# Kernel tuning notes

Hardware: AMD Instinct MI355X
Metric: run time of the kernel (lower is better)

The kernel has to match this reference:

```python
import jax, jax.numpy as jnp
import numpy as np

LATENT = 64

def _linear(x, W, b):
    return x @ W.T + b

def setup_inputs() -> dict:
    key = jax.random.key(0)
    ks = jax.random.split(key, 16)
    B, D, H, L = 16384, 784, 1024, LATENT
    def u(k, shape, fan_in):
        bound = 1.0 / np.sqrt(fan_in)
        return jax.random.uniform(k, shape, jnp.float32, -bound, bound)
    inp = {
        "x": jax.random.uniform(ks[0], (B, D), jnp.float32),
        "epsilon": jax.random.normal(ks[1], (B, L), jnp.float32),
        "W_ih": u(ks[2], (H, D), D), "b_ih": u(ks[3], (H,), D),
        "W_m":  u(ks[4], (L, H), H), "b_m":  u(ks[5], (L,), H),
        "W_lv": u(ks[6], (L, H), H), "b_lv": u(ks[7], (L,), H),
        "W_ap": u(ks[8], (L, H), H), "b_ap": u(ks[9], (L,), H),
        "W_lh": u(ks[10], (H, L), L), "b_lh": u(ks[11], (H,), L),
        "W_ho": u(ks[12], (D, H), H), "b_ho": u(ks[13], (D,), H),
    }
    return inp

def reference(x, epsilon, W_ih, b_ih, W_m, b_m, W_lv, b_lv, W_ap, b_ap, W_lh, b_lh, W_ho, b_ho):
    # ----- encode -----
    hidden = jnp.tanh(_linear(x, W_ih, b_ih))            # [B,H]
    mean   = _linear(hidden, W_m, b_m)                   # [B,L]
    logvar = jnp.clip(_linear(hidden, W_lv, b_lv), -4.5, 0.0)  # Hardtanh(-4.5,0)
    approx = _linear(hidden, W_ap, b_ap)                 # [B,L]
    # ----- reparameterize (rank-1 Gaussian) -----
    # inv_cov = diag(exp(logvar)) + approx approx^T   per sample
    B, L = mean.shape
    eye = jnp.eye(L, dtype=mean.dtype)
    inv_cov = jnp.exp(logvar)[:, :, None] * eye + approx[:, :, None] * approx[:, None, :]  # [B,L,L]
    cov = jnp.linalg.inv(inv_cov)                        # batched 64x64 inverse
    # torch.potrf default returns UPPER Cholesky U with U^T U = cov -> U = chol(cov).T
    Sigma = jnp.swapaxes(jnp.linalg.cholesky(cov), -1, -2)  # [B,L,L] upper
    z = mean + jnp.einsum('bij,bj->bi', Sigma, epsilon)  # [B,L]
    # ----- decode -----
    h2 = jnp.tanh(_linear(z, W_lh, b_lh))
    x_mean = jax.nn.sigmoid(_linear(h2, W_ho, b_ho))     # [B,784]
    return (x_mean, z, mean, logvar, approx)
```

## Files before the change

### kernel.cpp

```cpp
#include <hip/hip_runtime.h>
#include <hip/hip_bf16.h>
#include <math.h>

typedef __attribute__((ext_vector_type(8))) short short8;
typedef __attribute__((ext_vector_type(4))) float f32x4;
typedef __attribute__((ext_vector_type(4))) unsigned short us4;

#define GLOBAL_AS __attribute__((address_space(1)))
#define LDS_AS __attribute__((address_space(3)))

__device__ inline void g2l16(const void* g, void* l) {
    __builtin_amdgcn_global_load_lds((const GLOBAL_AS void*)g, (LDS_AS void*)l, 16, 0, 0);
}

__device__ inline unsigned short f2bf(float f) {
    unsigned int u = __float_as_uint(f);
    return (unsigned short)((u + 0x7fffu + ((u >> 16) & 1u)) >> 16);
}

template <int EPI>
__global__ __launch_bounds__(512, 2) void mgemm8(
    const __hip_bfloat16* __restrict__ A,
    const __hip_bfloat16* __restrict__ W,
    const float* __restrict__ bias,
    void* __restrict__ outp,
    int lda, int ldb, int nT, int ldc, int Nreal)
{
    __shared__ __align__(16) __hip_bfloat16 sh[2][32768];

    const int tid  = threadIdx.x;
    const int wave = tid >> 6;
    const int lane = tid & 63;
    const int rBase = blockIdx.x * 256;
    const int cBase = blockIdx.y * 256;

    const __hip_bfloat16* Ab = A + (size_t)rBase * lda;
    const __hip_bfloat16* Wb = W + (size_t)cBase * ldb;

    const int wr = (wave >> 2) * 128;
    const int wc = (wave & 3) * 64;
    const int h  = lane >> 4;
    const int r0 = lane & 15;
    const int swz = h ^ ((r0 >> 1) & 3);

    f32x4 acc[8][4];
#pragma unroll
    for (int m = 0; m < 8; ++m)
#pragma unroll
        for (int n = 0; n < 4; ++n) acc[m][n] = (f32x4){0.f, 0.f, 0.f, 0.f};

    auto stage_half = [&](int bb, int t, int ks) {
        const int k0 = t * 64 + ks * 32;
#pragma unroll
        for (int r = 0; r < 2; ++r) {
            int s2  = r * 512 + tid;
            int row = s2 >> 2;
            int cg  = (s2 & 3) ^ ((row >> 1) & 3);
            g2l16(Ab + (size_t)row * lda + k0 + cg * 8,
                  &sh[bb][(ks * 1024 + s2) * 8]);
            g2l16(Wb + (size_t)row * ldb + k0 + cg * 8,
                  &sh[bb][16384 + (ks * 1024 + s2) * 8]);
        }
    };

    auto phase = [&](int bb, int ks) {
        const __hip_bfloat16* base = &sh[bb][ks * 1024 * 8];
        short8 a_[8], b_[4];
#pragma unroll
        for (int i = 0; i < 8; ++i) {
            int R = wr + i * 16 + r0;
            a_[i] = *(const short8*)(base + (R * 4 + swz) * 8);
        }
#pragma unroll
        for (int j = 0; j < 4; ++j) {
            int R = wc + j * 16 + r0;
            b_[j] = *(const short8*)(base + 16384 + (R * 4 + swz) * 8);
        }
        __builtin_amdgcn_s_setprio(1);
#pragma unroll
        for (int i = 0; i < 8; ++i)
#pragma unroll
            for (int j = 0; j < 4; ++j)
                acc[i][j] = __builtin_amdgcn_mfma_f32_16x16x32_bf16(a_[i], b_[j], acc[i][j], 0, 0, 0);
        __builtin_amdgcn_s_setprio(0);
    };

    stage_half(0, 0, 0);
    stage_half(0, 0, 1);
    stage_half(1, 1, 0);
    for (int t = 0; t < nT; ++t) {
        const int cur = t & 1;
        if (t + 1 < nT) asm volatile("s_waitcnt vmcnt(8)" ::: "memory");
        else            asm volatile("s_waitcnt vmcnt(4)" ::: "memory");
        __builtin_amdgcn_s_barrier();
        if (t + 1 < nT) stage_half(cur ^ 1, t + 1, 1);
        phase(cur, 0);
        if (t + 1 < nT) asm volatile("s_waitcnt vmcnt(8)" ::: "memory");
        else            asm volatile("s_waitcnt vmcnt(0)" ::: "memory");
        __builtin_amdgcn_s_barrier();
        if (t + 2 < nT) stage_half(cur, t + 2, 0);
        phase(cur, 1);
    }

    const int rq = lane >> 4;
    const int c0 = lane & 15;
#pragma unroll
    for (int m = 0; m < 8; ++m) {
#pragma unroll
        for (int n = 0; n < 4; ++n) {
            f32x4 v = acc[m][n];
            const int gc = cBase + wc + n * 16 + c0;
            const float bv = bias[gc];
#pragma unroll
            for (int j = 0; j < 4; ++j) {
                const int gr = rBase + wr + m * 16 + rq * 4 + j;
                float val = v[j] + bv;
                if (EPI == 1) {
                    ((__hip_bfloat16*)outp)[(size_t)gr * ldc + gc] = __float2bfloat16(tanhf(val));
                } else {
                    if (gc < Nreal)
                        ((float*)outp)[(size_t)gr * Nreal + gc] = 1.f / (1.f + expf(-val));
                }
            }
        }
    }
}

template <int EPI>
__global__ __launch_bounds__(256) void mgemm(
    const __hip_bfloat16* __restrict__ A,
    const __hip_bfloat16* __restrict__ W,
    const float* __restrict__ bias,
    void* __restrict__ outp,
    int lda, int ldb, int nT, int ldc, int Nreal)
{
    __shared__ __align__(16) __hip_bfloat16 sh[2][8192];

    const int tid  = threadIdx.x;
    const int wave = tid >> 6;
    const int lane = tid & 63;
    const int rBase = blockIdx.x * 128;
    const int cBase = blockIdx.y * 128;

    const __hip_bfloat16* Ab = A + (size_t)rBase * lda;
    const __hip_bfloat16* Wb = W + (size_t)cBase * ldb;

    const int wr = (wave >> 1) * 64;
    const int wc = (wave & 1) * 64;
    const int h  = lane >> 4;
    const int r0 = lane & 15;
    const int swz = h ^ ((r0 >> 1) & 3);

    f32x4 acc[4][4];
#pragma unroll
    for (int m = 0; m < 4; ++m)
#pragma unroll
        for (int n = 0; n < 4; ++n) acc[m][n] = (f32x4){0.f, 0.f, 0.f, 0.f};

    auto stage = [&](int bb, int k0) {
#pragma unroll
        for (int r = 0; r < 2; ++r) {
            int s2  = r * 256 + tid;
            int row = s2 >> 2;
            int cg  = (s2 & 3) ^ ((row >> 1) & 3);
            g2l16(Ab + (size_t)row * lda + k0 + cg * 8, &sh[bb][s2 * 8]);
            g2l16(Wb + (size_t)row * ldb + k0 + cg * 8, &sh[bb][4096 + s2 * 8]);
        }
    };

    auto compute = [&](int bb) {
        const __hip_bfloat16* base = &sh[bb][0];
        short8 a_[4], b_[4];
#pragma unroll
        for (int m = 0; m < 4; ++m) {
            int R = wr + m * 16 + r0;
            a_[m] = *(const short8*)(base + (R * 4 + swz) * 8);
        }
#pragma unroll
        for (int n = 0; n < 4; ++n) {
            int R = wc + n * 16 + r0;
            b_[n] = *(const short8*)(base + 4096 + (R * 4 + swz) * 8);
        }
#pragma unroll
        for (int m = 0; m < 4; ++m)
#pragma unroll
            for (int n = 0; n < 4; ++n)
                acc[m][n] = __builtin_amdgcn_mfma_f32_16x16x32_bf16(a_[m], b_[n], acc[m][n], 0, 0, 0);
    };

    stage(0, 0);
    __syncthreads();
    int cur = 0;
    for (int t = 0; t < nT; ++t) {
        if (t + 1 < nT) stage(cur ^ 1, (t + 1) * 32);
        compute(cur);
        __syncthreads();
        cur ^= 1;
    }

    const int rq = lane >> 4;
    const int c0 = lane & 15;
#pragma unroll
    for (int m = 0; m < 4; ++m) {
#pragma unroll
        for (int n = 0; n < 4; ++n) {
            f32x4 v = acc[m][n];
            const int gc = cBase + wc + n * 16 + c0;
            const float bv = bias[gc];
#pragma unroll
            for (int j = 0; j < 4; ++j) {
                const int gr = rBase + wr + m * 16 + rq * 4 + j;
                float val = v[j] + bv;
                if (EPI == 0) {
                    const int sel = gc >> 6, cc = gc & 63;
                    if (sel < 3) {
                        if (sel == 1) val = fminf(fmaxf(val, -4.5f), 0.f);
                        ((float*)outp)[(size_t)sel * (16384u * 64u) + (size_t)gr * 64 + cc] = val;
                    }
                } else if (EPI == 1) {
                    ((__hip_bfloat16*)outp)[(size_t)gr * ldc + gc] = __float2bfloat16(tanhf(val));
                }
            }
        }
    }
}

__global__ void cvt_pad4(const float* __restrict__ src, unsigned short* __restrict__ dst,
                         int scols, int dcols, long total4)
{
    long i = (long)blockIdx.x * 256 + threadIdx.x;
    if (i >= total4) return;
    long e = i * 4;
    long row = e / dcols;
    int  c = (int)(e - row * dcols);
    us4 o = (us4){0, 0, 0, 0};
    if (c < scols) {
        float4 v = *(const float4*)(src + row * (long)scols + c);
        o.x = f2bf(v.x); o.y = f2bf(v.y); o.z = f2bf(v.z); o.w = f2bf(v.w);
    }
    *(us4*)(dst + e) = o;
}

__global__ void cvt_rows4(const float* __restrict__ src, unsigned short* __restrict__ dst,
                          int srows, long total4)
{
    long i = (long)blockIdx.x * 256 + threadIdx.x;
    if (i >= total4) return;
    long e = i * 4;
    int r = (int)(e >> 10), c = (int)(e & 1023);
    us4 o = (us4){0, 0, 0, 0};
    if (r < srows) {
        float4 v = *(const float4*)(src + (size_t)r * 1024 + c);
        o.x = f2bf(v.x); o.y = f2bf(v.y); o.z = f2bf(v.z); o.w = f2bf(v.w);
    }
    *(us4*)(dst + e) = o;
}

__global__ void pack_heads(const float* __restrict__ Wm, const float* __restrict__ Wlv,
                           const float* __restrict__ Wap, __hip_bfloat16* __restrict__ dst)
{
    int i = blockIdx.x * 256 + threadIdx.x;
    int r = i >> 10, c = i & 1023;
    float v = 0.f;
    if (r < 64)       v = Wm[(size_t)r * 1024 + c];
    else if (r < 128) v = Wlv[(size_t)(r - 64) * 1024 + c];
    else if (r < 192) v = Wap[(size_t)(r - 128) * 1024 + c];
    dst[i] = __float2bfloat16(v);
}

__global__ void pack_bias3(const float* bm, const float* blv, const float* bap, float* dst)
{
    int i = threadIdx.x;
    float v = 0.f;
    if (i < 64)       v = bm[i];
    else if (i < 128) v = blv[i - 64];
    else if (i < 192) v = bap[i - 128];
    dst[i] = v;
}

__global__ void pad_vec(const float* src, float* dst, int n, int total)
{
    int i = blockIdx.x * 256 + threadIdx.x;
    if (i >= total) return;
    dst[i] = (i < n) ? src[i] : 0.f;
}

__global__ __launch_bounds__(256) void reparam_kernel(
    const float* __restrict__ mean, const float* __restrict__ logvar,
    const float* __restrict__ approx, const float* __restrict__ eps,
    float* __restrict__ z, __hip_bfloat16* __restrict__ zb, int B)
{
    const int gid  = blockIdx.x * 256 + threadIdx.x;
    const int row  = gid >> 6;
    const int lane = threadIdx.x & 63;
    if (row >= B) return;

    const size_t idx = (size_t)row * 64 + lane;
    const float m  = mean[idx];
    const float lv = logvar[idx];
    const float a  = approx[idx];
    const float ep = eps[idx];

    const float s  = expf(-lv);
    const float x1 = a * a * s;
    const float x2 = s * a * ep;

    float R = x1, S = x2;
#pragma unroll
    for (int off = 1; off < 64; off <<= 1) {
        float r2 = __shfl_down(R, off, 64);
        float s2 = __shfl_down(S, off, 64);
        if (lane + off < 64) { R += r2; S += s2; }
    }
    const float Rexc  = R - x1;
    const float Sexc  = S - x2;
    const float inv1R = 1.f / (1.f + R);
    const float dL    = sqrtf(s * (1.f + Rexc) * inv1R);
    const float bj    = -s * a * inv1R / dL;

    const float zv = m + dL * ep + bj * Sexc;
    z[idx]  = zv;
    zb[idx] = __float2bfloat16(zv);
}

extern "C" void kernel_launch(void* const* d_in, const int* in_sizes, int n_in,
                              void* d_out, int out_size, void* d_ws, size_t ws_size,
                              hipStream_t stream)
{
    const float* x    = (const float*)d_in[0];
    const float* eps  = (const float*)d_in[1];
    const float* W_ih = (const float*)d_in[2];
    const float* b_ih = (const float*)d_in[3];
    const float* W_m  = (const float*)d_in[4];
    const float* b_m  = (const float*)d_in[5];
    const float* W_lv = (const float*)d_in[6];
    const float* b_lv = (const float*)d_in[7];
    const float* W_ap = (const float*)d_in[8];
    const float* b_ap = (const float*)d_in[9];
    const float* W_lh = (const float*)d_in[10];
    const float* b_lh = (const float*)d_in[11];
    const float* W_ho = (const float*)d_in[12];
    const float* b_ho = (const float*)d_in[13];

    const int B = 16384;

    float* out    = (float*)d_out;
    float* x_mean = out;
    float* z      = out + (size_t)B * 784;
    float* mean   = z + (size_t)B * 64;
    float* logvar = mean + (size_t)B * 64;
    float* approx = logvar + (size_t)B * 64;

    char* ws = (char*)d_ws;
    __hip_bfloat16* hb    = (__hip_bfloat16*)(ws + 0);
    __hip_bfloat16* xb    = (__hip_bfloat16*)(ws + 33554432);
    __hip_bfloat16* wihb  = (__hip_bfloat16*)(ws + 60817408);
    __hip_bfloat16* whead = (__hip_bfloat16*)(ws + 62521344);
    __hip_bfloat16* wlhb  = (__hip_bfloat16*)(ws + 63045632);
    __hip_bfloat16* whob  = (__hip_bfloat16*)(ws + 63176704);
    float*          bhead = (float*)(ws + 65273856);
    float*          bho   = (float*)(ws + 65274880);
    __hip_bfloat16* h2b   = hb;
    __hip_bfloat16* zb    = xb;

    long g;
    g = (long)B * 832 / 4;
    cvt_pad4<<<dim3((g + 255) / 256), dim3(256), 0, stream>>>(x, (unsigned short*)xb, 784, 832, g);
    g = 1024L * 832 / 4;
    cvt_pad4<<<dim3((g + 255) / 256), dim3(256), 0, stream>>>(W_ih, (unsigned short*)wihb, 784, 832, g);
    pack_heads<<<dim3(1024), dim3(256), 0, stream>>>(W_m, W_lv, W_ap, whead);
    pack_bias3<<<dim3(1), dim3(256), 0, stream>>>(b_m, b_lv, b_ap, bhead);
    g = 1024L * 64 / 4;
    cvt_pad4<<<dim3((g + 255) / 256), dim3(256), 0, stream>>>(W_lh, (unsigned short*)wlhb, 64, 64, g);
    g = 1024L * 1024 / 4;
    cvt_rows4<<<dim3((g + 255) / 256), dim3(256), 0, stream>>>(W_ho, (unsigned short*)whob, 784, g);
    pad_vec<<<dim3(4), dim3(256), 0, stream>>>(b_ho, bho, 784, 1024);

    mgemm8<1><<<dim3(64, 4), dim3(512), 0, stream>>>(xb, wihb, b_ih, hb, 832, 832, 13, 1024, 1024);

    mgemm<0><<<dim3(128, 2), dim3(256), 0, stream>>>(hb, whead, bhead, mean, 1024, 1024, 32, 0, 192);

    reparam_kernel<<<dim3((B * 64) / 256), dim3(256), 0, stream>>>(mean, logvar, approx, eps, z, zb, B);

    mgemm<1><<<dim3(128, 8), dim3(256), 0, stream>>>(zb, wlhb, b_lh, h2b, 64, 64, 2, 1024, 1024);

    mgemm8<2><<<dim3(64, 4), dim3(512), 0, stream>>>(h2b, whob, bho, x_mean, 1024, 1024, 16, 784, 784);
}
```

Baseline: 167.0 us.

## Shrink GEMM tiles to 256x128 with K=32 stages and trim decoder padding

Replaces the 256x256, K=64 split-phase GEMM with a 256x128 tile using K=32 double-buffered stages, 8 waves each computing 64x64, and launch bounds allowing 4 blocks per CU. The decoder output GEMM now pads N to 896 instead of 1024, using 7 column blocks, which avoids wasted work on padded columns. The aim is better occupancy and less padding waste. In exchange, each tile reuses less data from LDS and the pipeline gains an extra barrier per iteration.

After: 160.5 us. -3.9%, faster.

```diff
diff --git a/kernel.cpp b/kernel.cpp
--- a/kernel.cpp
+++ b/kernel.cpp
@@ -19,93 +19,91 @@
 }
 
 template <int EPI>
-__global__ __launch_bounds__(512, 2) void mgemm8(
+__global__ __launch_bounds__(512, 4) void mgemmB(
     const __hip_bfloat16* __restrict__ A,
     const __hip_bfloat16* __restrict__ W,
     const float* __restrict__ bias,
     void* __restrict__ outp,
     int lda, int ldb, int nT, int ldc, int Nreal)
 {
-    __shared__ __align__(16) __hip_bfloat16 sh[2][32768];
+    __shared__ __align__(16) __hip_bfloat16 sh[2][12288];
 
     const int tid  = threadIdx.x;
     const int wave = tid >> 6;
     const int lane = tid & 63;
     const int rBase = blockIdx.x * 256;
-    const int cBase = blockIdx.y * 256;
+    const int cBase = blockIdx.y * 128;
 
     const __hip_bfloat16* Ab = A + (size_t)rBase * lda;
     const __hip_bfloat16* Wb = W + (size_t)cBase * ldb;
 
-    const int wr = (wave >> 2) * 128;
-    const int wc = (wave & 3) * 64;
+    const int wr = (wave >> 1) * 64;
+    const int wc = (wave & 1) * 64;
     const int h  = lane >> 4;
     const int r0 = lane & 15;
     const int swz = h ^ ((r0 >> 1) & 3);
 
-    f32x4 acc[8][4];
-#pragma unroll
-    for (int m = 0; m < 8; ++m)
+    f32x4 acc[4][4];
+#pragma unroll
+    for (int m = 0; m < 4; ++m)
 #pragma unroll
         for (int n = 0; n < 4; ++n) acc[m][n] = (f32x4){0.f, 0.f, 0.f, 0.f};
 
-    auto stage_half = [&](int bb, int t, int ks) {
-        const int k0 = t * 64 + ks * 32;
+    auto stage = [&](int bb, int t) {
+        const int k0 = t * 32;
 #pragma unroll
         for (int r = 0; r < 2; ++r) {
             int s2  = r * 512 + tid;
             int row = s2 >> 2;
             int cg  = (s2 & 3) ^ ((row >> 1) & 3);
-            g2l16(Ab + (size_t)row * lda + k0 + cg * 8,
-                  &sh[bb][(ks * 1024 + s2) * 8]);
-            g2l16(Wb + (size_t)row * ldb + k0 + cg * 8,
-                  &sh[bb][16384 + (ks * 1024 + s2) * 8]);
+            g2l16(Ab + (size_t)row * lda + k0 + cg * 8, &sh[bb][s2 * 8]);
+        }
+        {
+            int s2  = tid;
+            int row = s2 >> 2;
+            int cg  = (s2 & 3) ^ ((row >> 1) & 3);
+            g2l16(Wb + (size_t)row * ldb + k0 + cg * 8, &sh[bb][8192 + s2 * 8]);
         }
     };
 
-    auto phase = [&](int bb, int ks) {
-        const __hip_bfloat16* base = &sh[bb][ks * 1024 * 8];
-        short8 a_[8], b_[4];
-#pragma unroll
-        for (int i = 0; i < 8; ++i) {
-            int R = wr + i * 16 + r0;
-            a_[i] = *(const short8*)(base + (R * 4 + swz) * 8);
-        }
-#pragma unroll
-        for (int j = 0; j < 4; ++j) {
-            int R = wc + j * 16 + r0;
-            b_[j] = *(const short8*)(base + 16384 + (R * 4 + swz) * 8);
+    auto compute = [&](int bb) {
+        const __hip_bfloat16* base = &sh[bb][0];
+        short8 a_[4], b_[4];
+#pragma unroll
+        for (int m = 0; m < 4; ++m) {
+            int R = wr + m * 16 + r0;
+            a_[m] = *(const short8*)(base + (R * 4 + swz) * 8);
+        }
+#pragma unroll
+        for (int n = 0; n < 4; ++n) {
+            int R = wc + n * 16 + r0;
+            b_[n] = *(const short8*)(base + 8192 + (R * 4 + swz) * 8);
         }
         __builtin_amdgcn_s_setprio(1);
 #pragma unroll
-        for (int i = 0; i < 8; ++i)
-#pragma unroll
-            for (int j = 0; j < 4; ++j)
-                acc[i][j] = __builtin_amdgcn_mfma_f32_16x16x32_bf16(a_[i], b_[j], acc[i][j], 0, 0, 0);
+        for (int m = 0; m < 4; ++m)
+#pragma unroll
+            for (int n = 0; n < 4; ++n)
+                acc[m][n] = __builtin_amdgcn_mfma_f32_16x16x32_bf16(a_[m], b_[n], acc[m][n], 0, 0, 0);
         __builtin_amdgcn_s_setprio(0);
     };
 
-    stage_half(0, 0, 0);
-    stage_half(0, 0, 1);
-    stage_half(1, 1, 0);
+    stage(0, 0);
+    stage(1, 1);
     for (int t = 0; t < nT; ++t) {
         const int cur = t & 1;
-        if (t + 1 < nT) asm volatile("s_waitcnt vmcnt(8)" ::: "memory");
-        else            asm volatile("s_waitcnt vmcnt(4)" ::: "memory");
-        __builtin_amdgcn_s_barrier();
-        if (t + 1 < nT) stage_half(cur ^ 1, t + 1, 1);
-        phase(cur, 0);
-        if (t + 1 < nT) asm volatile("s_waitcnt vmcnt(8)" ::: "memory");
+        if (t + 1 < nT) asm volatile("s_waitcnt vmcnt(3)" ::: "memory");
         else            asm volatile("s_waitcnt vmcnt(0)" ::: "memory");
         __builtin_amdgcn_s_barrier();
-        if (t + 2 < nT) stage_half(cur, t + 2, 0);
-        phase(cur, 1);
+        compute(cur);
+        __builtin_amdgcn_s_barrier();
+        if (t + 2 < nT) stage(cur, t + 2);
     }
 
     const int rq = lane >> 4;
     const int c0 = lane & 15;
 #pragma unroll
-    for (int m = 0; m < 8; ++m) {
+    for (int m = 0; m < 4; ++m) {
 #pragma unroll
         for (int n = 0; n < 4; ++n) {
             f32x4 v = acc[m][n];
@@ -372,11 +370,11 @@
     pack_bias3<<<dim3(1), dim3(256), 0, stream>>>(b_m, b_lv, b_ap, bhead);
     g = 1024L * 64 / 4;
     cvt_pad4<<<dim3((g + 255) / 256), dim3(256), 0, stream>>>(W_lh, (unsigned short*)wlhb, 64, 64, g);
-    g = 1024L * 1024 / 4;
+    g = 896L * 1024 / 4;
     cvt_rows4<<<dim3((g + 255) / 256), dim3(256), 0, stream>>>(W_ho, (unsigned short*)whob, 784, g);
-    pad_vec<<<dim3(4), dim3(256), 0, stream>>>(b_ho, bho, 784, 1024);
-
-    mgemm8<1><<<dim3(64, 4), dim3(512), 0, stream>>>(xb, wihb, b_ih, hb, 832, 832, 13, 1024, 1024);
+    pad_vec<<<dim3(4), dim3(256), 0, stream>>>(b_ho, bho, 784, 896);
+
+    mgemmB<1><<<dim3(64, 8), dim3(512), 0, stream>>>(xb, wihb, b_ih, hb, 832, 832, 26, 1024, 1024);
 
     mgemm<0><<<dim3(128, 2), dim3(256), 0, stream>>>(hb, whead, bhead, mean, 1024, 1024, 32, 0, 192);
 
@@ -384,5 +382,5 @@
 
     mgemm<1><<<dim3(128, 8), dim3(256), 0, stream>>>(zb, wlhb, b_lh, h2b, 64, 64, 2, 1024, 1024);
 
-    mgemm8<2><<<dim3(64, 4), dim3(512), 0, stream>>>(h2b, whob, bho, x_mean, 1024, 1024, 16, 784, 784);
-}
+    mgemmB<2><<<dim3(64, 7), dim3(512), 0, stream>>>(h2b, whob, bho, x_mean, 1024, 1024, 32, 784, 784);
+}
```

## Interleave LDS reads, async loads and MFMA in finer phases; fuse prep kernels

Applied to the files above, without the earlier changes.

The big GEMM main loop is restructured into eight sub-phases per two k-tiles. In each, A/B fragments are read from LDS in halves, the next global-to-LDS loads are issued, and MFMAs run on half the B columns, with barriers between phases. This aims to hide LDS and global latency behind matrix ops and to cut register pressure, since b_ now holds 2 fragments instead of 4. Seven small conversion and packing launches become two fused prep kernels. K is padded to 896 so the tile count is even, which adds a little wasted MFMA work for the first GEMM. The loop assumes nT is even, and the extra barriers add sync cost.

After: 158.4 us. 1.05x faster.

```diff
diff --git a/kernel.cpp b/kernel.cpp
--- a/kernel.cpp
+++ b/kernel.cpp
@@ -18,8 +18,11 @@
     return (unsigned short)((u + 0x7fffu + ((u >> 16) & 1u)) >> 16);
 }
 
+#define FENCE asm volatile("" ::: "memory")
+#define BAR __builtin_amdgcn_s_barrier()
+
 template <int EPI>
-__global__ __launch_bounds__(512, 2) void mgemm8(
+__global__ __launch_bounds__(512, 2) void mgemmP(
     const __hip_bfloat16* __restrict__ A,
     const __hip_bfloat16* __restrict__ W,
     const float* __restrict__ bias,
@@ -49,57 +52,88 @@
 #pragma unroll
         for (int n = 0; n < 4; ++n) acc[m][n] = (f32x4){0.f, 0.f, 0.f, 0.f};
 
-    auto stage_half = [&](int bb, int t, int ks) {
-        const int k0 = t * 64 + ks * 32;
+    auto qA = [&](int t, int ks) {
+        if (t >= nT) return;
+        const int bb = t & 1, k0 = t * 64 + ks * 32;
 #pragma unroll
         for (int r = 0; r < 2; ++r) {
-            int s2  = r * 512 + tid;
-            int row = s2 >> 2;
-            int cg  = (s2 & 3) ^ ((row >> 1) & 3);
-            g2l16(Ab + (size_t)row * lda + k0 + cg * 8,
-                  &sh[bb][(ks * 1024 + s2) * 8]);
-            g2l16(Wb + (size_t)row * ldb + k0 + cg * 8,
-                  &sh[bb][16384 + (ks * 1024 + s2) * 8]);
-        }
-    };
-
-    auto phase = [&](int bb, int ks) {
-        const __hip_bfloat16* base = &sh[bb][ks * 1024 * 8];
-        short8 a_[8], b_[4];
+            int s2 = r * 512 + tid, row = s2 >> 2, cg = (s2 & 3) ^ ((row >> 1) & 3);
+            g2l16(Ab + (size_t)row * lda + k0 + cg * 8, &sh[bb][(ks * 1024 + s2) * 8]);
+        }
+    };
+    auto qB = [&](int t, int ks) {
+        if (t >= nT) return;
+        const int bb = t & 1, k0 = t * 64 + ks * 32;
+#pragma unroll
+        for (int r = 0; r < 2; ++r) {
+            int s2 = r * 512 + tid, row = s2 >> 2, cg = (s2 & 3) ^ ((row >> 1) & 3);
+            g2l16(Wb + (size_t)row * ldb + k0 + cg * 8, &sh[bb][16384 + (ks * 1024 + s2) * 8]);
+        }
+    };
+
+    short8 a_[8], b_[2];
+    auto dsA = [&](int bb, int ks) {
+        const __hip_bfloat16* base = &sh[bb][ks * 8192];
 #pragma unroll
         for (int i = 0; i < 8; ++i) {
             int R = wr + i * 16 + r0;
             a_[i] = *(const short8*)(base + (R * 4 + swz) * 8);
         }
-#pragma unroll
-        for (int j = 0; j < 4; ++j) {
-            int R = wc + j * 16 + r0;
-            b_[j] = *(const short8*)(base + 16384 + (R * 4 + swz) * 8);
-        }
+    };
+    auto dsB = [&](int bb, int ks, int nh) {
+        const __hip_bfloat16* base = &sh[bb][16384 + ks * 8192];
+#pragma unroll
+        for (int j = 0; j < 2; ++j) {
+            int R = wc + (nh * 2 + j) * 16 + r0;
+            b_[j] = *(const short8*)(base + (R * 4 + swz) * 8);
+        }
+    };
+    auto mma = [&](int nh) {
         __builtin_amdgcn_s_setprio(1);
 #pragma unroll
         for (int i = 0; i < 8; ++i)
 #pragma unroll
-            for (int j = 0; j < 4; ++j)
-                acc[i][j] = __builtin_amdgcn_mfma_f32_16x16x32_bf16(a_[i], b_[j], acc[i][j], 0, 0, 0);
+            for (int j = 0; j < 2; ++j)
+                acc[i][nh * 2 + j] = __builtin_amdgcn_mfma_f32_16x16x32_bf16(
+                    a_[i], b_[j], acc[i][nh * 2 + j], 0, 0, 0);
         __builtin_amdgcn_s_setprio(0);
     };
 
-    stage_half(0, 0, 0);
-    stage_half(0, 0, 1);
-    stage_half(1, 1, 0);
-    for (int t = 0; t < nT; ++t) {
-        const int cur = t & 1;
-        if (t + 1 < nT) asm volatile("s_waitcnt vmcnt(8)" ::: "memory");
-        else            asm volatile("s_waitcnt vmcnt(4)" ::: "memory");
-        __builtin_amdgcn_s_barrier();
-        if (t + 1 < nT) stage_half(cur ^ 1, t + 1, 1);
-        phase(cur, 0);
-        if (t + 1 < nT) asm volatile("s_waitcnt vmcnt(8)" ::: "memory");
-        else            asm volatile("s_waitcnt vmcnt(0)" ::: "memory");
-        __builtin_amdgcn_s_barrier();
-        if (t + 2 < nT) stage_half(cur, t + 2, 0);
-        phase(cur, 1);
+    qA(0, 0); qB(0, 0); qA(0, 1); qB(0, 1); qA(1, 0); qB(1, 0); qA(1, 1);
+    asm volatile("s_waitcnt vmcnt(6)" ::: "memory");
+    FENCE; BAR; FENCE;
+
+    const int nIter = nT >> 1;
+    for (int it = 0; it < nIter; ++it) {
+        const int T0 = 2 * it, T1 = 2 * it + 1;
+        const bool lastIt = (it == nIter - 1);
+        dsA(0, 0); dsB(0, 0, 0); qB(T1, 1);
+        mma(0);
+        FENCE; BAR; FENCE;
+        dsB(0, 0, 1); qA(T0 + 2, 0);
+        mma(1);
+        FENCE; BAR; FENCE;
+        dsA(0, 1); dsB(0, 1, 0); qB(T0 + 2, 0);
+        mma(0);
+        FENCE; BAR; FENCE;
+        dsB(0, 1, 1); qA(T0 + 2, 1);
+        mma(1);
+        if (lastIt) asm volatile("s_waitcnt vmcnt(0)" ::: "memory");
+        else        asm volatile("s_waitcnt vmcnt(6)" ::: "memory");
+        FENCE; BAR; FENCE;
+        dsA(1, 0); dsB(1, 0, 0); qB(T0 + 2, 1);
+        mma(0);
+        FENCE; BAR; FENCE;
+        dsB(1, 0, 1); qA(T1 + 2, 0);
+        mma(1);
+        FENCE; BAR; FENCE;
+        dsA(1, 1); dsB(1, 1, 0); qB(T1 + 2, 0);
+        mma(0);
+        FENCE; BAR; FENCE;
+        dsB(1, 1, 1); qA(T1 + 2, 1);
+        mma(1);
+        if (!lastIt) asm volatile("s_waitcnt vmcnt(6)" ::: "memory");
+        FENCE; BAR; FENCE;
     }
 
     const int rq = lane >> 4;
@@ -225,64 +259,82 @@
     }
 }
 
-__global__ void cvt_pad4(const float* __restrict__ src, unsigned short* __restrict__ dst,
-                         int scols, int dcols, long total4)
-{
-    long i = (long)blockIdx.x * 256 + threadIdx.x;
-    if (i >= total4) return;
-    long e = i * 4;
-    long row = e / dcols;
-    int  c = (int)(e - row * dcols);
-    us4 o = (us4){0, 0, 0, 0};
-    if (c < scols) {
-        float4 v = *(const float4*)(src + row * (long)scols + c);
+__global__ void prep1(const float* __restrict__ x, const float* __restrict__ Wih,
+                      const float* __restrict__ Wm, const float* __restrict__ Wlv,
+                      const float* __restrict__ Wap, const float* __restrict__ bm,
+                      const float* __restrict__ blv, const float* __restrict__ bap,
+                      const float* __restrict__ bho_src,
+                      unsigned short* __restrict__ xw,
+                      unsigned short* __restrict__ whead,
+                      float* __restrict__ bhead, float* __restrict__ bho)
+{
+    const long SEG0 = 17408L * 224, SEG1 = SEG0 + 65536, SEG2 = SEG1 + 64, SEG3 = SEG2 + 256;
+    long u = (long)blockIdx.x * 256 + threadIdx.x;
+    if (u < SEG0) {
+        long r = u / 224;
+        int  c = (int)(u - r * 224) * 4;
+        us4 o = (us4){0, 0, 0, 0};
+        if (c < 784) {
+            const float* src = (r < 16384) ? (x + r * 784) : (Wih + (r - 16384) * 784);
+            float4 v = *(const float4*)(src + c);
+            o.x = f2bf(v.x); o.y = f2bf(v.y); o.z = f2bf(v.z); o.w = f2bf(v.w);
+        }
+        *(us4*)(xw + r * 896 + c) = o;
+    } else if (u < SEG1) {
+        long t = u - SEG0;
+        int r = (int)(t >> 8), c = (int)(t & 255) * 4;
+        us4 o = (us4){0, 0, 0, 0};
+        const float* src = nullptr;
+        if (r < 64)       src = Wm + (size_t)r * 1024;
+        else if (r < 128) src = Wlv + (size_t)(r - 64) * 1024;
+        else if (r < 192) src = Wap + (size_t)(r - 128) * 1024;
+        if (src) {
+            float4 v = *(const float4*)(src + c);
+            o.x = f2bf(v.x); o.y = f2bf(v.y); o.z = f2bf(v.z); o.w = f2bf(v.w);
+        }
+        *(us4*)(whead + (size_t)r * 1024 + c) = o;
+    } else if (u < SEG2) {
+        int base = (int)(u - SEG1) * 4;
+#pragma unroll
+        for (int k = 0; k < 4; ++k) {
+            int p = base + k;
+            float v = 0.f;
+            if (p < 64)       v = bm[p];
+            else if (p < 128) v = blv[p - 64];
+            else if (p < 192) v = bap[p - 128];
+            bhead[p] = v;
+        }
+    } else if (u < SEG3) {
+        int base = (int)(u - SEG2) * 4;
+#pragma unroll
+        for (int k = 0; k < 4; ++k) {
+            int p = base + k;
+            bho[p] = (p < 784) ? bho_src[p] : 0.f;
+        }
+    }
+}
+
+__global__ void prep2(const float* __restrict__ Who, const float* __restrict__ Wlh,
+                      unsigned short* __restrict__ whob, unsigned short* __restrict__ wlhb)
+{
+    const long SEG0 = 262144, SEG1 = SEG0 + 16384;
+    long u = (long)blockIdx.x * 256 + threadIdx.x;
+    if (u < SEG0) {
+        int r = (int)(u >> 8), c = (int)(u & 255) * 4;
+        us4 o = (us4){0, 0, 0, 0};
+        if (r < 784) {
+            float4 v = *(const float4*)(Who + (size_t)r * 1024 + c);
+            o.x = f2bf(v.x); o.y = f2bf(v.y); o.z = f2bf(v.z); o.w = f2bf(v.w);
+        }
+        *(us4*)(whob + (size_t)r * 1024 + c) = o;
+    } else if (u < SEG1) {
+        long t = u - SEG0;
+        int r = (int)(t >> 4), c = (int)(t & 15) * 4;
+        float4 v = *(const float4*)(Wlh + (size_t)r * 64 + c);
+        us4 o;
         o.x = f2bf(v.x); o.y = f2bf(v.y); o.z = f2bf(v.z); o.w = f2bf(v.w);
-    }
-    *(us4*)(dst + e) = o;
-}
-
-__global__ void cvt_rows4(const float* __restrict__ src, unsigned short* __restrict__ dst,
-                          int srows, long total4)
-{
-    long i = (long)blockIdx.x * 256 + threadIdx.x;
-    if (i >= total4) return;
-    long e = i * 4;
-    int r = (int)(e >> 10), c = (int)(e & 1023);
-    us4 o = (us4){0, 0, 0, 0};
-    if (r < srows) {
-        float4 v = *(const float4*)(src + (size_t)r * 1024 + c);
-        o.x = f2bf(v.x); o.y = f2bf(v.y); o.z = f2bf(v.z); o.w = f2bf(v.w);
-    }
-    *(us4*)(dst + e) = o;
-}
-
-__global__ void pack_heads(const float* __restrict__ Wm, const float* __restrict__ Wlv,
-                           const float* __restrict__ Wap, __hip_bfloat16* __restrict__ dst)
-{
-    int i = blockIdx.x * 256 + threadIdx.x;
-    int r = i >> 10, c = i & 1023;
-    float v = 0.f;
-    if (r < 64)       v = Wm[(size_t)r * 1024 + c];
-    else if (r < 128) v = Wlv[(size_t)(r - 64) * 1024 + c];
-    else if (r < 192) v = Wap[(size_t)(r - 128) * 1024 + c];
-    dst[i] = __float2bfloat16(v);
-}
-
-__global__ void pack_bias3(const float* bm, const float* blv, const float* bap, float* dst)
-{
-    int i = threadIdx.x;
-    float v = 0.f;
-    if (i < 64)       v = bm[i];
-    else if (i < 128) v = blv[i - 64];
-    else if (i < 192) v = bap[i - 128];
-    dst[i] = v;
-}
-
-__global__ void pad_vec(const float* src, float* dst, int n, int total)
-{
-    int i = blockIdx.x * 256 + threadIdx.x;
-    if (i >= total) return;
-    dst[i] = (i < n) ? src[i] : 0.f;
+        *(us4*)(wlhb + (size_t)r * 64 + c) = o;
+    }
 }
 
 __global__ __launch_bounds__(256) void reparam_kernel(
@@ -354,29 +406,26 @@
     char* ws = (char*)d_ws;
     __hip_bfloat16* hb    = (__hip_bfloat16*)(ws + 0);
     __hip_bfloat16* xb    = (__hip_bfloat16*)(ws + 33554432);
-    __hip_bfloat16* wihb  = (__hip_bfloat16*)(ws + 60817408);
-    __hip_bfloat16* whead = (__hip_bfloat16*)(ws + 62521344);
-    __hip_bfloat16* wlhb  = (__hip_bfloat16*)(ws + 63045632);
-    __hip_bfloat16* whob  = (__hip_bfloat16*)(ws + 63176704);
+    __hip_bfloat16* wihb  = (__hip_bfloat16*)(ws + 62914560);
+    __hip_bfloat16* whead = (__hip_bfloat16*)(ws + 64749568);
     float*          bhead = (float*)(ws + 65273856);
     float*          bho   = (float*)(ws + 65274880);
+    __hip_bfloat16* zb    = (__hip_bfloat16*)(ws + 33554432);
+    __hip_bfloat16* whob  = (__hip_bfloat16*)(ws + 37748736);
+    __hip_bfloat16* wlhb  = (__hip_bfloat16*)(ws + 39845888);
     __hip_bfloat16* h2b   = hb;
-    __hip_bfloat16* zb    = xb;
-
-    long g;
-    g = (long)B * 832 / 4;
-    cvt_pad4<<<dim3((g + 255) / 256), dim3(256), 0, stream>>>(x, (unsigned short*)xb, 784, 832, g);
-    g = 1024L * 832 / 4;
-    cvt_pad4<<<dim3((g + 255) / 256), dim3(256), 0, stream>>>(W_ih, (unsigned short*)wihb, 784, 832, g);
-    pack_heads<<<dim3(1024), dim3(256), 0, stream>>>(W_m, W_lv, W_ap, whead);
-    pack_bias3<<<dim3(1), dim3(256), 0, stream>>>(b_m, b_lv, b_ap, bhead);
-    g = 1024L * 64 / 4;
-    cvt_pad4<<<dim3((g + 255) / 256), dim3(256), 0, stream>>>(W_lh, (unsigned short*)wlhb, 64, 64, g);
-    g = 1024L * 1024 / 4;
-    cvt_rows4<<<dim3((g + 255) / 256), dim3(256), 0, stream>>>(W_ho, (unsigned short*)whob, 784, g);
-    pad_vec<<<dim3(4), dim3(256), 0, stream>>>(b_ho, bho, 784, 1024);
-
-    mgemm8<1><<<dim3(64, 4), dim3(512), 0, stream>>>(xb, wihb, b_ih, hb, 832, 832, 13, 1024, 1024);
+
+    {
+        long total = 17408L * 224 + 65536 + 64 + 256;
+        prep1<<<dim3((total + 255) / 256), dim3(256), 0, stream>>>(
+            x, W_ih, W_m, W_lv, W_ap, b_m, b_lv, b_ap, b_ho,
+            (unsigned short*)xb, (unsigned short*)whead, bhead, bho);
+    }
+
+    mgemmP<1><<<dim3(64, 4), dim3(512), 0, stream>>>(xb, wihb, b_ih, hb, 896, 896, 14, 1024, 1024);
+
+    prep2<<<dim3((262144 + 16384 + 255) / 256), dim3(256), 0, stream>>>(
+        W_ho, W_lh, (unsigned short*)whob, (unsigned short*)wlhb);
 
     mgemm<0><<<dim3(128, 2), dim3(256), 0, stream>>>(hb, whead, bhead, mean, 1024, 1024, 32, 0, 192);
 
@@ -384,5 +433,5 @@
 
     mgemm<1><<<dim3(128, 8), dim3(256), 0, stream>>>(zb, wlhb, b_lh, h2b, 64, 64, 2, 1024, 1024);
 
-    mgemm8<2><<<dim3(64, 4), dim3(512), 0, stream>>>(h2b, whob, bho, x_mean, 1024, 1024, 16, 784, 784);
-}
+    mgemmP<2><<<dim3(64, 4), dim3(512), 0, stream>>>(h2b, whob, bho, x_mean, 1024, 1024, 16, 784, 784);
+}
```
